# Performance work log

Hardware: AMD Instinct MI355X
Metric: run time of the kernel (lower is better)

Reference implementation:

```python
import jax, jax.numpy as jnp
import numpy as np

B, T, I = 2048, 256, 64
XH, G, Hd, O = 128, 64, 64, 24
DT = 1.0  # delta_t; with unit-spaced times -> exactly one Euler step per observation


def setup_inputs() -> dict:
    key = jax.random.key(0)
    ks = jax.random.split(key, 16)
    s = 0.05
    return {
        "H": jax.random.normal(ks[0], (B, T, I), jnp.float32),
        "times": jnp.arange(T, dtype=jnp.int64 if jax.config.jax_enable_x64 else jnp.int32).reshape(1, T),
        # x_model: Linear(I->XH), ReLU, Linear(XH->G)
        "W1": jax.random.normal(ks[1], (XH, I), jnp.float32) * s,
        "b1": jax.random.normal(ks[2], (XH,), jnp.float32) * s,
        "W2": jax.random.normal(ks[3], (G, XH), jnp.float32) * s,
        "b2": jax.random.normal(ks[4], (G,), jnp.float32) * s,
        # autonomous GRU-ODE cell (no bias)
        "Whr": jax.random.normal(ks[5], (Hd, Hd), jnp.float32) * s,
        "Whz": jax.random.normal(ks[6], (Hd, Hd), jnp.float32) * s,
        "Whh": jax.random.normal(ks[7], (Hd, Hd), jnp.float32) * s,
        # nn.GRU (single layer), PyTorch gate order [r, z, n]
        "w_ih": jax.random.normal(ks[8], (3 * Hd, G), jnp.float32) * s,
        "w_hh": jax.random.normal(ks[9], (3 * Hd, Hd), jnp.float32) * s,
        "b_ih": jax.random.normal(ks[10], (3 * Hd,), jnp.float32) * s,
        "b_hh": jax.random.normal(ks[11], (3 * Hd,), jnp.float32) * s,
        # rec_linear: Linear(G->O)
        "Wr": jax.random.normal(ks[12], (O, G), jnp.float32) * s,
        "br": jax.random.normal(ks[13], (O,), jnp.float32) * s,
    }


def _forward(H, W1, b1, W2, b2, Whr, Whz, Whh, w_ih, w_hh, b_ih, b_hh, Wr, br):
    # x_model: [B,T,I] -> [B,T,G]
    HH = jnp.maximum(H @ W1.T + b1, 0.0) @ W2.T + b2

    def step(h, x_t):
        # one Euler GRU-ODE step (autonomous cell, x=0)
        r = jax.nn.sigmoid(h @ Whr.T)
        z = jax.nn.sigmoid(h @ Whz.T)
        u = jnp.tanh((r * h) @ Whh.T)
        h = h + DT * (1.0 - z) * (u - h)
        # GRU observation cell (PyTorch semantics, gate order r,z,n)
        gi = x_t @ w_ih.T + b_ih
        gh = h @ w_hh.T + b_hh
        i_r, i_z, i_n = jnp.split(gi, 3, axis=-1)
        h_r, h_z, h_n = jnp.split(gh, 3, axis=-1)
        r2 = jax.nn.sigmoid(i_r + h_r)
        z2 = jax.nn.sigmoid(i_z + h_z)
        n = jnp.tanh(i_n + r2 * h_n)
        h_new = (1.0 - z2) * n + z2 * h
        return h_new, h_new  # GRU output == new hidden for single layer

    h0 = jnp.zeros((HH.shape[0], Hd), HH.dtype)
    _, outs = jax.lax.scan(step, h0, jnp.swapaxes(HH, 0, 1))  # [T,B,Hd]
    out = jnp.swapaxes(outs, 0, 1)  # [B,T,Hd] (Hd == G)
    return out @ Wr.T + br  # identity last activation


def reference(H, times, W1, b1, W2, b2, Whr, Whz, Whh, w_ih, w_hh, b_ih, b_hh, Wr, br):
    # times = arange(T) with delta_t=1 -> exactly one ODE step per observation
    return _forward(H, W1, b1, W2, b2, Whr, Whz, Whh, w_ih, w_hh, b_ih, b_hh, Wr, br)
```

## Files before the change

### kernel.cpp

```cpp
#include <hip/hip_runtime.h>
#include <hip/hip_bf16.h>


#define T_STEPS 256

typedef short bf16x8 __attribute__((ext_vector_type(8)));
typedef short short4v __attribute__((ext_vector_type(4)));
typedef float f32x4 __attribute__((ext_vector_type(4)));

#define MFMA(a, b, c) __builtin_amdgcn_mfma_f32_16x16x32_bf16((a), (b), (c), 0, 0, 0)

__device__ __forceinline__ void barrier_lds() {
  asm volatile("s_waitcnt lgkmcnt(0)\n\ts_barrier" ::: "memory");
}

__device__ __forceinline__ short f2bf(float f) {
  __hip_bfloat16 b = __float2bfloat16(f);
  return __builtin_bit_cast(short, b);
}

__device__ __forceinline__ f32x4 sigm4(f32x4 x) {
  f32x4 r;
#pragma unroll
  for (int j = 0; j < 4; ++j) {
    float e = __builtin_amdgcn_exp2f(-1.442695041f * x[j]);
    r[j] = __builtin_amdgcn_rcpf(1.f + e);
  }
  return r;
}
__device__ __forceinline__ f32x4 tanh4(f32x4 x) {
  f32x4 r;
#pragma unroll
  for (int j = 0; j < 4; ++j) {
    float e = __builtin_amdgcn_exp2f(2.885390082f * x[j]);
    r[j] = 1.f - 2.f * __builtin_amdgcn_rcpf(1.f + e);
  }
  return r;
}
__device__ __forceinline__ short4v cvt4(f32x4 v) {
  short4v p;
#pragma unroll
  for (int j = 0; j < 4; ++j) p[j] = f2bf(v[j]);
  return p;
}
__device__ __forceinline__ void split_store(char* phi, char* plo, f32x4 v) {
  unsigned u0 = __builtin_bit_cast(unsigned, v[0]);
  unsigned u1 = __builtin_bit_cast(unsigned, v[1]);
  unsigned u2 = __builtin_bit_cast(unsigned, v[2]);
  unsigned u3 = __builtin_bit_cast(unsigned, v[3]);
  float l0 = v[0] - __builtin_bit_cast(float, u0 & 0xFFFF0000u);
  float l1 = v[1] - __builtin_bit_cast(float, u1 & 0xFFFF0000u);
  float l2 = v[2] - __builtin_bit_cast(float, u2 & 0xFFFF0000u);
  float l3 = v[3] - __builtin_bit_cast(float, u3 & 0xFFFF0000u);
  uint2 hi, lo;
  hi.x = __builtin_amdgcn_perm(u1, u0, 0x07060302u);
  hi.y = __builtin_amdgcn_perm(u3, u2, 0x07060302u);
  lo.x = __builtin_amdgcn_perm(__builtin_bit_cast(unsigned, l1),
                               __builtin_bit_cast(unsigned, l0), 0x07060302u);
  lo.y = __builtin_amdgcn_perm(__builtin_bit_cast(unsigned, l3),
                               __builtin_bit_cast(unsigned, l2), 0x07060302u);
  *(uint2*)phi = hi;
  *(uint2*)plo = lo;
}
__device__ __forceinline__ bf16x8 wfrag(const float* __restrict__ W, int stride, int row, int c0) {
  const float* p = W + (size_t)row * stride + c0;
  float4 a = *(const float4*)p;
  float4 b = *(const float4*)(p + 4);
  bf16x8 r;
  r[0] = f2bf(a.x); r[1] = f2bf(a.y); r[2] = f2bf(a.z); r[3] = f2bf(a.w);
  r[4] = f2bf(b.x); r[5] = f2bf(b.y); r[6] = f2bf(b.z); r[7] = f2bf(b.w);
  return r;
}

__device__ __forceinline__ int swz64(int row, int off) { return row * 128 + (off ^ ((row & 7) << 4)); }
__device__ __forceinline__ int swzH(int row, int off)  { return row * 256 + (off ^ ((row & 7) << 4)); }

__global__ __launch_bounds__(512, 1) void odegru(
    const float* __restrict__ H,
    const float* __restrict__ W1, const float* __restrict__ b1,
    const float* __restrict__ W2, const float* __restrict__ b2,
    const float* __restrict__ Wor, const float* __restrict__ Woz, const float* __restrict__ Woh,
    const float* __restrict__ wih, const float* __restrict__ whhg,
    const float* __restrict__ bih, const float* __restrict__ bhh,
    const float* __restrict__ Wr, const float* __restrict__ br,
    float* __restrict__ out) {
  const int tid = threadIdx.x;
  const int w = tid >> 6;
  const int l = tid & 63;
  const int col = l & 15;
  const int g = l >> 4;
  const int b0 = blockIdx.x << 4;
  const bool helper = (w >= 4);
  const int hw = w - 4;
  const f32x4 zero4 = {0.f, 0.f, 0.f, 0.f};

  __shared__ __align__(16) char sm[30720];
  char* HIDb = sm;
  char* XGb  = sm + 4096;
  char* Hhi  = sm + 6144;
  char* Hlo  = sm + 8192;
  char* RHhi = sm + 10240;
  char* RHlo = sm + 12288;
  char* H2hi = sm + 14336;
  char* H2lo = sm + 16384;
  char* GIb  = sm + 18432;

  ((long long*)Hhi)[tid] = 0;

  const int row4 = 16 * (helper ? hw : w) + 4 * g;
  const int r16 = 16 * (helper ? hw : w) + col;
  const int sR0 = swz64(col, 16 * g);
  const int sR1 = swz64(col, 64 + 16 * g);
  const int sW  = swz64(col, row4 * 2);

  bf16x8 aR0, aR1, aZ0, aZ1, aU0, aU1, aHR0, aHR1, aHZ0, aHZ1, aHN0, aHN1;
  f32x4 bhn;
  bf16x8 aW1_00, aW1_01, aW1_10, aW1_11, aW2_0, aW2_1, aW2_2, aW2_3;
  bf16x8 aIR0, aIR1, aIZ0, aIZ1, aIN0, aIN1, aWr0, aWr1;
  f32x4 bsr, bsz, bin_, b1a, b1b, b2w, brw;
  const float* xp = nullptr;
  float4 xa, xb, xc, xd;
  float* outp = nullptr;
  int sHid0, sHid1, sHid2, sHid3, sHidW0, sHidW1, giW;
  const int giR = (w * 64 + l) * 16;

  if (!helper) {
    aR0 = wfrag(Wor, 64, r16, 8 * g);          aR1 = wfrag(Wor, 64, r16, 32 + 8 * g);
    aZ0 = wfrag(Woz, 64, r16, 8 * g);          aZ1 = wfrag(Woz, 64, r16, 32 + 8 * g);
    aU0 = wfrag(Woh, 64, r16, 8 * g);          aU1 = wfrag(Woh, 64, r16, 32 + 8 * g);
    aHR0 = wfrag(whhg, 64, r16, 8 * g);        aHR1 = wfrag(whhg, 64, r16, 32 + 8 * g);
    aHZ0 = wfrag(whhg, 64, 64 + r16, 8 * g);   aHZ1 = wfrag(whhg, 64, 64 + r16, 32 + 8 * g);
    aHN0 = wfrag(whhg, 64, 128 + r16, 8 * g);  aHN1 = wfrag(whhg, 64, 128 + r16, 32 + 8 * g);
#pragma unroll
    for (int j = 0; j < 4; ++j) bhn[j] = bhh[128 + row4 + j];
  } else {
    aW1_00 = wfrag(W1, 64, r16, 8 * g);        aW1_01 = wfrag(W1, 64, r16, 32 + 8 * g);
    aW1_10 = wfrag(W1, 64, 64 + r16, 8 * g);   aW1_11 = wfrag(W1, 64, 64 + r16, 32 + 8 * g);
    aW2_0 = wfrag(W2, 128, r16, 8 * g);        aW2_1 = wfrag(W2, 128, r16, 32 + 8 * g);
    aW2_2 = wfrag(W2, 128, r16, 64 + 8 * g);   aW2_3 = wfrag(W2, 128, r16, 96 + 8 * g);
    aIR0 = wfrag(wih, 64, r16, 8 * g);         aIR1 = wfrag(wih, 64, r16, 32 + 8 * g);
    aIZ0 = wfrag(wih, 64, 64 + r16, 8 * g);    aIZ1 = wfrag(wih, 64, 64 + r16, 32 + 8 * g);
    aIN0 = wfrag(wih, 64, 128 + r16, 8 * g);   aIN1 = wfrag(wih, 64, 128 + r16, 32 + 8 * g);
    const int wr_row = r16 > 23 ? 23 : r16;
    aWr0 = wfrag(Wr, 64, wr_row, 8 * g);       aWr1 = wfrag(Wr, 64, wr_row, 32 + 8 * g);
#pragma unroll
    for (int j = 0; j < 4; ++j) {
      bsr[j] = bih[row4 + j] + bhh[row4 + j];
      bsz[j] = bih[64 + row4 + j] + bhh[64 + row4 + j];
      bin_[j] = bih[128 + row4 + j];
      b1a[j] = b1[row4 + j];
      b1b[j] = b1[64 + row4 + j];
      b2w[j] = b2[row4 + j];
      int o = row4 + j;
      brw[j] = br[o > 23 ? 23 : o];
    }
    sHid0 = swzH(col, 16 * g);
    sHid1 = swzH(col, 64 + 16 * g);
    sHid2 = swzH(col, 128 + 16 * g);
    sHid3 = swzH(col, 192 + 16 * g);
    sHidW0 = swzH(col, row4 * 2);
    sHidW1 = swzH(col, (64 + row4) * 2);
    giW = (hw * 64 + l) * 16;
    xp = H + ((size_t)(b0 + col) * T_STEPS) * 64 + 8 * g;
    xa = *(const float4*)(xp);      xb = *(const float4*)(xp + 4);
    xc = *(const float4*)(xp + 32); xd = *(const float4*)(xp + 36);
    outp = out + ((size_t)(b0 + col) * T_STEPS) * 24 + row4;
  }

  f32x4 hreg = {0.f, 0.f, 0.f, 0.f};

  if (helper) {
    bf16x8 xB0, xB1;
    xB0[0] = f2bf(xa.x); xB0[1] = f2bf(xa.y); xB0[2] = f2bf(xa.z); xB0[3] = f2bf(xa.w);
    xB0[4] = f2bf(xb.x); xB0[5] = f2bf(xb.y); xB0[6] = f2bf(xb.z); xB0[7] = f2bf(xb.w);
    xB1[0] = f2bf(xc.x); xB1[1] = f2bf(xc.y); xB1[2] = f2bf(xc.z); xB1[3] = f2bf(xc.w);
    xB1[4] = f2bf(xd.x); xB1[5] = f2bf(xd.y); xB1[6] = f2bf(xd.z); xB1[7] = f2bf(xd.w);
    f32x4 hid0 = MFMA(aW1_00, xB0, b1a), hid0b = MFMA(aW1_01, xB1, zero4);
    f32x4 hid1 = MFMA(aW1_10, xB0, b1b), hid1b = MFMA(aW1_11, xB1, zero4);
    hid0 += hid0b; hid1 += hid1b;
#pragma unroll
    for (int j = 0; j < 4; ++j) { hid0[j] = fmaxf(hid0[j], 0.f); hid1[j] = fmaxf(hid1[j], 0.f); }
    *(short4v*)(HIDb + sHidW0) = cvt4(hid0);
    *(short4v*)(HIDb + sHidW1) = cvt4(hid1);
  }
  barrier_lds();
  if (helper) {
    bf16x8 hdB0 = *(const bf16x8*)(HIDb + sHid0);
    bf16x8 hdB1 = *(const bf16x8*)(HIDb + sHid1);
    bf16x8 hdB2 = *(const bf16x8*)(HIDb + sHid2);
    bf16x8 hdB3 = *(const bf16x8*)(HIDb + sHid3);
    f32x4 x0 = MFMA(aW2_0, hdB0, b2w),  x1 = MFMA(aW2_1, hdB1, zero4);
    f32x4 x2 = MFMA(aW2_2, hdB2, zero4), x3 = MFMA(aW2_3, hdB3, zero4);
    *(short4v*)(XGb + sW) = cvt4((x0 + x1) + (x2 + x3));
    xp += 64;
    xa = *(const float4*)(xp);      xb = *(const float4*)(xp + 4);
    xc = *(const float4*)(xp + 32); xd = *(const float4*)(xp + 36);
  }
  barrier_lds();

  for (int t = 0; t < T_STEPS; ++t) {
    if (helper) {
      bf16x8 xgB0 = *(const bf16x8*)(XGb + sR0);
      bf16x8 xgB1 = *(const bf16x8*)(XGb + sR1);
      f32x4 gr0 = MFMA(aIR0, xgB0, bsr),  gr1 = MFMA(aIR1, xgB1, zero4);
      f32x4 gz0 = MFMA(aIZ0, xgB0, bsz),  gz1 = MFMA(aIZ1, xgB1, zero4);
      f32x4 gn0 = MFMA(aIN0, xgB0, bin_), gn1 = MFMA(aIN1, xgB1, zero4);
      *(f32x4*)(GIb + 0 * 4096 + giW) = gr0 + gr1;
      *(f32x4*)(GIb + 1 * 4096 + giW) = gz0 + gz1;
      *(f32x4*)(GIb + 2 * 4096 + giW) = gn0 + gn1;
      barrier_lds();
      if (hw < 2 && t > 0) {
        bf16x8 hB0h = *(const bf16x8*)(Hhi + sR0);
        bf16x8 hB1h = *(const bf16x8*)(Hhi + sR1);
        bf16x8 hB0l = *(const bf16x8*)(Hlo + sR0);
        bf16x8 hB1l = *(const bf16x8*)(Hlo + sR1);
        f32x4 a5 = MFMA(aWr0, hB0h, brw),   a5b = MFMA(aWr1, hB1h, zero4);
        f32x4 a5l = MFMA(aWr0, hB0l, zero4), a5lb = MFMA(aWr1, hB1l, zero4);
        a5 = (a5 + a5b) + (a5l + a5lb);
        if (hw == 0 || g < 2) { outp[0] = a5[0]; outp[1] = a5[1]; outp[2] = a5[2]; outp[3] = a5[3]; }
        outp += 24;
      }
      if (t + 1 < T_STEPS) {
        bf16x8 xB0, xB1;
        xB0[0] = f2bf(xa.x); xB0[1] = f2bf(xa.y); xB0[2] = f2bf(xa.z); xB0[3] = f2bf(xa.w);
        xB0[4] = f2bf(xb.x); xB0[5] = f2bf(xb.y); xB0[6] = f2bf(xb.z); xB0[7] = f2bf(xb.w);
        xB1[0] = f2bf(xc.x); xB1[1] = f2bf(xc.y); xB1[2] = f2bf(xc.z); xB1[3] = f2bf(xc.w);
        xB1[4] = f2bf(xd.x); xB1[5] = f2bf(xd.y); xB1[6] = f2bf(xd.z); xB1[7] = f2bf(xd.w);
        if (t + 2 < T_STEPS) {
          xp += 64;
          xa = *(const float4*)(xp);      xb = *(const float4*)(xp + 4);
          xc = *(const float4*)(xp + 32); xd = *(const float4*)(xp + 36);
        }
        f32x4 hid0 = MFMA(aW1_00, xB0, b1a), hid0b = MFMA(aW1_01, xB1, zero4);
        f32x4 hid1 = MFMA(aW1_10, xB0, b1b), hid1b = MFMA(aW1_11, xB1, zero4);
        hid0 += hid0b; hid1 += hid1b;
#pragma unroll
        for (int j = 0; j < 4; ++j) { hid0[j] = fmaxf(hid0[j], 0.f); hid1[j] = fmaxf(hid1[j], 0.f); }
        *(short4v*)(HIDb + sHidW0) = cvt4(hid0);
        *(short4v*)(HIDb + sHidW1) = cvt4(hid1);
      }
      barrier_lds();
      if (t + 1 < T_STEPS) {
        bf16x8 hdB0 = *(const bf16x8*)(HIDb + sHid0);
        bf16x8 hdB1 = *(const bf16x8*)(HIDb + sHid1);
        bf16x8 hdB2 = *(const bf16x8*)(HIDb + sHid2);
        bf16x8 hdB3 = *(const bf16x8*)(HIDb + sHid3);
        f32x4 x0 = MFMA(aW2_0, hdB0, b2w),   x1 = MFMA(aW2_1, hdB1, zero4);
        f32x4 x2 = MFMA(aW2_2, hdB2, zero4), x3 = MFMA(aW2_3, hdB3, zero4);
        *(short4v*)(XGb + sW) = cvt4((x0 + x1) + (x2 + x3));
      }
      barrier_lds();
    } else {
      __builtin_amdgcn_s_setprio(1);
      bf16x8 hB0h = *(const bf16x8*)(Hhi + sR0);
      bf16x8 hB1h = *(const bf16x8*)(Hhi + sR1);
      bf16x8 hB0l = *(const bf16x8*)(Hlo + sR0);
      bf16x8 hB1l = *(const bf16x8*)(Hlo + sR1);
      f32x4 r00 = MFMA(aR0, hB0h, zero4), r10 = MFMA(aR1, hB1h, zero4);
      f32x4 r01 = MFMA(aR0, hB0l, zero4), r11 = MFMA(aR1, hB1l, zero4);
      f32x4 z00 = MFMA(aZ0, hB0h, zero4), z10 = MFMA(aZ1, hB1h, zero4);
      f32x4 z01 = MFMA(aZ0, hB0l, zero4), z11 = MFMA(aZ1, hB1l, zero4);
      f32x4 rr = sigm4((r00 + r10) + (r01 + r11));
      split_store(RHhi + sW, RHlo + sW, rr * hreg);
      f32x4 zz = sigm4((z00 + z10) + (z01 + z11));
      barrier_lds();
      bf16x8 rhB0h = *(const bf16x8*)(RHhi + sR0);
      bf16x8 rhB1h = *(const bf16x8*)(RHhi + sR1);
      bf16x8 rhB0l = *(const bf16x8*)(RHlo + sR0);
      bf16x8 rhB1l = *(const bf16x8*)(RHlo + sR1);
      f32x4 gir = *(const f32x4*)(GIb + 0 * 4096 + giR);
      f32x4 giz = *(const f32x4*)(GIb + 1 * 4096 + giR);
      f32x4 gin = *(const f32x4*)(GIb + 2 * 4096 + giR);
      f32x4 u00 = MFMA(aU0, rhB0h, zero4), u10 = MFMA(aU1, rhB1h, zero4);
      f32x4 u01 = MFMA(aU0, rhB0l, zero4), u11 = MFMA(aU1, rhB1l, zero4);
      f32x4 uu = tanh4((u00 + u10) + (u01 + u11));
      f32x4 hp = uu - zz * (uu - hreg);
      split_store(H2hi + sW, H2lo + sW, hp);
      barrier_lds();
      bf16x8 h2B0h = *(const bf16x8*)(H2hi + sR0);
      bf16x8 h2B1h = *(const bf16x8*)(H2hi + sR1);
      bf16x8 h2B0l = *(const bf16x8*)(H2lo + sR0);
      bf16x8 h2B1l = *(const bf16x8*)(H2lo + sR1);
      f32x4 hr00 = MFMA(aHR0, h2B0h, zero4), hr10 = MFMA(aHR1, h2B1h, zero4);
      f32x4 hr01 = MFMA(aHR0, h2B0l, zero4), hr11 = MFMA(aHR1, h2B1l, zero4);
      f32x4 hn00 = MFMA(aHN0, h2B0h, bhn),   hn10 = MFMA(aHN1, h2B1h, zero4);
      f32x4 hn01 = MFMA(aHN0, h2B0l, zero4), hn11 = MFMA(aHN1, h2B1l, zero4);
      f32x4 hz00 = MFMA(aHZ0, h2B0h, zero4), hz10 = MFMA(aHZ1, h2B1h, zero4);
      f32x4 hz01 = MFMA(aHZ0, h2B0l, zero4), hz11 = MFMA(aHZ1, h2B1l, zero4);
      f32x4 r2 = sigm4(gir + (hr00 + hr10) + (hr01 + hr11));
      f32x4 nn = tanh4(gin + r2 * ((hn00 + hn10) + (hn01 + hn11)));
      f32x4 z2 = sigm4(giz + (hz00 + hz10) + (hz01 + hz11));
      hreg = nn + z2 * (hp - nn);
      split_store(Hhi + sW, Hlo + sW, hreg);
      __builtin_amdgcn_s_setprio(0);
      barrier_lds();
    }
  }

  if (helper && hw < 2) {
    bf16x8 hB0h = *(const bf16x8*)(Hhi + sR0);
    bf16x8 hB1h = *(const bf16x8*)(Hhi + sR1);
    bf16x8 hB0l = *(const bf16x8*)(Hlo + sR0);
    bf16x8 hB1l = *(const bf16x8*)(Hlo + sR1);
    f32x4 a5 = MFMA(aWr0, hB0h, brw),   a5b = MFMA(aWr1, hB1h, zero4);
    f32x4 a5l = MFMA(aWr0, hB0l, zero4), a5lb = MFMA(aWr1, hB1l, zero4);
    a5 = (a5 + a5b) + (a5l + a5lb);
    if (hw == 0 || g < 2) { outp[0] = a5[0]; outp[1] = a5[1]; outp[2] = a5[2]; outp[3] = a5[3]; }
  }
}

extern "C" void kernel_launch(void* const* d_in, const int* in_sizes, int n_in,
                              void* d_out, int out_size, void* d_ws, size_t ws_size,
                              hipStream_t stream) {
  (void)in_sizes; (void)n_in; (void)d_ws; (void)ws_size; (void)out_size;
  const float* H   = (const float*)d_in[0];
  const float* W1  = (const float*)d_in[2];
  const float* b1  = (const float*)d_in[3];
  const float* W2  = (const float*)d_in[4];
  const float* b2  = (const float*)d_in[5];
  const float* Whr = (const float*)d_in[6];
  const float* Whz = (const float*)d_in[7];
  const float* Whh = (const float*)d_in[8];
  const float* wih = (const float*)d_in[9];
  const float* whh = (const float*)d_in[10];
  const float* bih = (const float*)d_in[11];
  const float* bhh = (const float*)d_in[12];
  const float* Wr  = (const float*)d_in[13];
  const float* br  = (const float*)d_in[14];
  float* out = (float*)d_out;

  odegru<<<dim3(2048 / 16), dim3(512), 0, stream>>>(
      H, W1, b1, W2, b2, Whr, Whz, Whh, wih, whh, bih, bhh, Wr, br, out);
}
```

Baseline: 368.9 us.

## Double-buffer hidden state so helper output projection runs later in step

The hidden state buffer is double-buffered, with read and write pointers swapped each step. The helper warps' output projection (Wr matmul and global store) can then move after the x_model work, reading the previous step's buffer instead of racing the main warps' write. This takes the output work off the helper's early critical phase between barriers. It also moves the r-gate sigmoid and store ahead of the z-gate MFMAs so the RH store is issued earlier, at the cost of 4 KB more LDS.

```diff
diff --git a/kernel.cpp b/kernel.cpp
--- a/kernel.cpp
+++ b/kernel.cpp
@@ -94,18 +94,24 @@
   const int hw = w - 4;
   const f32x4 zero4 = {0.f, 0.f, 0.f, 0.f};
 
-  __shared__ __align__(16) char sm[30720];
+  __shared__ __align__(16) char sm[34816];
   char* HIDb = sm;
   char* XGb  = sm + 4096;
-  char* Hhi  = sm + 6144;
-  char* Hlo  = sm + 8192;
+  char* Hhi0 = sm + 6144;
+  char* Hlo0 = sm + 8192;
   char* RHhi = sm + 10240;
   char* RHlo = sm + 12288;
   char* H2hi = sm + 14336;
   char* H2lo = sm + 16384;
   char* GIb  = sm + 18432;
-
-  ((long long*)Hhi)[tid] = 0;
+  char* Hhi1 = sm + 30720;
+  char* Hlo1 = sm + 32768;
+
+  ((long long*)Hhi0)[tid] = 0;
+  ((long long*)Hhi1)[tid] = 0;
+
+  char* HhiR = Hhi1; char* HloR = Hlo1;
+  char* HhiW = Hhi0; char* HloW = Hlo0;
 
   const int row4 = 16 * (helper ? hw : w) + 4 * g;
   const int r16 = 16 * (helper ? hw : w) + col;
@@ -209,17 +215,6 @@
       *(f32x4*)(GIb + 1 * 4096 + giW) = gz0 + gz1;
       *(f32x4*)(GIb + 2 * 4096 + giW) = gn0 + gn1;
       barrier_lds();
-      if (hw < 2 && t > 0) {
-        bf16x8 hB0h = *(const bf16x8*)(Hhi + sR0);
-        bf16x8 hB1h = *(const bf16x8*)(Hhi + sR1);
-        bf16x8 hB0l = *(const bf16x8*)(Hlo + sR0);
-        bf16x8 hB1l = *(const bf16x8*)(Hlo + sR1);
-        f32x4 a5 = MFMA(aWr0, hB0h, brw),   a5b = MFMA(aWr1, hB1h, zero4);
-        f32x4 a5l = MFMA(aWr0, hB0l, zero4), a5lb = MFMA(aWr1, hB1l, zero4);
-        a5 = (a5 + a5b) + (a5l + a5lb);
-        if (hw == 0 || g < 2) { outp[0] = a5[0]; outp[1] = a5[1]; outp[2] = a5[2]; outp[3] = a5[3]; }
-        outp += 24;
-      }
       if (t + 1 < T_STEPS) {
         bf16x8 xB0, xB1;
         xB0[0] = f2bf(xa.x); xB0[1] = f2bf(xa.y); xB0[2] = f2bf(xa.z); xB0[3] = f2bf(xa.w);
@@ -249,19 +244,30 @@
         f32x4 x2 = MFMA(aW2_2, hdB2, zero4), x3 = MFMA(aW2_3, hdB3, zero4);
         *(short4v*)(XGb + sW) = cvt4((x0 + x1) + (x2 + x3));
       }
+      if (hw < 2 && t > 0) {
+        bf16x8 hB0h = *(const bf16x8*)(HhiR + sR0);
+        bf16x8 hB1h = *(const bf16x8*)(HhiR + sR1);
+        bf16x8 hB0l = *(const bf16x8*)(HloR + sR0);
+        bf16x8 hB1l = *(const bf16x8*)(HloR + sR1);
+        f32x4 a5 = MFMA(aWr0, hB0h, brw),   a5b = MFMA(aWr1, hB1h, zero4);
+        f32x4 a5l = MFMA(aWr0, hB0l, zero4), a5lb = MFMA(aWr1, hB1l, zero4);
+        a5 = (a5 + a5b) + (a5l + a5lb);
+        if (hw == 0 || g < 2) { outp[0] = a5[0]; outp[1] = a5[1]; outp[2] = a5[2]; outp[3] = a5[3]; }
+        outp += 24;
+      }
       barrier_lds();
     } else {
       __builtin_amdgcn_s_setprio(1);
-      bf16x8 hB0h = *(const bf16x8*)(Hhi + sR0);
-      bf16x8 hB1h = *(const bf16x8*)(Hhi + sR1);
-      bf16x8 hB0l = *(const bf16x8*)(Hlo + sR0);
-      bf16x8 hB1l = *(const bf16x8*)(Hlo + sR1);
+      bf16x8 hB0h = *(const bf16x8*)(HhiR + sR0);
+      bf16x8 hB1h = *(const bf16x8*)(HhiR + sR1);
+      bf16x8 hB0l = *(const bf16x8*)(HloR + sR0);
+      bf16x8 hB1l = *(const bf16x8*)(HloR + sR1);
       f32x4 r00 = MFMA(aR0, hB0h, zero4), r10 = MFMA(aR1, hB1h, zero4);
       f32x4 r01 = MFMA(aR0, hB0l, zero4), r11 = MFMA(aR1, hB1l, zero4);
+      f32x4 rr = sigm4((r00 + r10) + (r01 + r11));
+      split_store(RHhi + sW, RHlo + sW, rr * hreg);
       f32x4 z00 = MFMA(aZ0, hB0h, zero4), z10 = MFMA(aZ1, hB1h, zero4);
       f32x4 z01 = MFMA(aZ0, hB0l, zero4), z11 = MFMA(aZ1, hB1l, zero4);
-      f32x4 rr = sigm4((r00 + r10) + (r01 + r11));
-      split_store(RHhi + sW, RHlo + sW, rr * hreg);
       f32x4 zz = sigm4((z00 + z10) + (z01 + z11));
       barrier_lds();
       bf16x8 rhB0h = *(const bf16x8*)(RHhi + sR0);
@@ -291,17 +297,19 @@
       f32x4 nn = tanh4(gin + r2 * ((hn00 + hn10) + (hn01 + hn11)));
       f32x4 z2 = sigm4(giz + (hz00 + hz10) + (hz01 + hz11));
       hreg = nn + z2 * (hp - nn);
-      split_store(Hhi + sW, Hlo + sW, hreg);
+      split_store(HhiW + sW, HloW + sW, hreg);
       __builtin_amdgcn_s_setprio(0);
       barrier_lds();
     }
+    char* t0 = HhiR; HhiR = HhiW; HhiW = t0;
+    char* t1 = HloR; HloR = HloW; HloW = t1;
   }
 
   if (helper && hw < 2) {
-    bf16x8 hB0h = *(const bf16x8*)(Hhi + sR0);
-    bf16x8 hB1h = *(const bf16x8*)(Hhi + sR1);
-    bf16x8 hB0l = *(const bf16x8*)(Hlo + sR0);
-    bf16x8 hB1l = *(const bf16x8*)(Hlo + sR1);
+    bf16x8 hB0h = *(const bf16x8*)(HhiR + sR0);
+    bf16x8 hB1h = *(const bf16x8*)(HhiR + sR1);
+    bf16x8 hB0l = *(const bf16x8*)(HloR + sR0);
+    bf16x8 hB1l = *(const bf16x8*)(HloR + sR1);
     f32x4 a5 = MFMA(aWr0, hB0h, brw),   a5b = MFMA(aWr1, hB1h, zero4);
     f32x4 a5l = MFMA(aWr0, hB0l, zero4), a5lb = MFMA(aWr1, hB1l, zero4);
     a5 = (a5 + a5b) + (a5l + a5lb);
```

New measurement: 333.9 us. -9.5%, faster.
